# Optimization experiments

Hardware: AMD Instinct MI355X
Metric: run time of the kernel (lower is better)

## Reference

```python
import jax, jax.numpy as jnp
import numpy as np
from jax import lax

B, H, W, C = 8, 64, 64, 256
OUT = 1024          # channels (final conv filters)
KS = 3              # kernel_size
GROUP_DIV = 1
N_GROUPS = C // GROUP_DIV  # 256 -> depthwise-style grouped convs
DN = ('NHWC', 'HWIO', 'NHWC')
EPS = 1e-5


def setup_inputs() -> dict:
    key = jax.random.key(0)
    ks = jax.random.split(key, 6)
    x = jax.random.normal(ks[0], (B, H, W, C), jnp.float32)
    w_spatial = jax.random.normal(ks[1], (B, KS, KS, C // N_GROUPS, C), jnp.float32) * 0.05
    w_pointwise = jax.random.normal(ks[2], (B, 1, 1, C // N_GROUPS, C), jnp.float32) * 0.05
    bias = jax.random.normal(ks[3], (B, C), jnp.float32) * 0.05
    conv_w = jax.random.normal(ks[4], (KS, KS, C, OUT), jnp.float32) * (1.0 / np.sqrt(KS * KS * C))
    conv_b = jnp.zeros((OUT,), jnp.float32)
    return {"x": x, "w_spatial": w_spatial, "w_pointwise": w_pointwise,
            "bias": bias, "conv_w": conv_w, "conv_b": conv_b}


def _instance_norm(x):
    # TF: (x - mean) / (std + eps), population std over H,W per sample/channel
    mean = jnp.mean(x, axis=(1, 2), keepdims=True)
    std = jnp.sqrt(jnp.mean((x - mean) ** 2, axis=(1, 2), keepdims=True))
    return (x - mean) / (std + EPS)


def _per_sample(xi, ws, wp, b):
    # xi: [H,W,C]; ws: [ks,ks,1,C]; wp: [1,1,1,C]; b: [C]
    y = lax.conv_general_dilated(xi[None], ws, (1, 1), 'SAME',
                                 dimension_numbers=DN,
                                 feature_group_count=N_GROUPS)
    y = lax.conv_general_dilated(y, wp, (1, 1), 'VALID',
                                 dimension_numbers=DN,
                                 feature_group_count=N_GROUPS) + b
    return y[0]


def reference(x, w_spatial, w_pointwise, bias, conv_w, conv_b):
    x = _instance_norm(x)
    # batched per-sample dynamic grouped spatial + pointwise conv
    x = jax.vmap(_per_sample)(x, w_spatial, w_pointwise, bias)  # [B,H,W,C]
    # shared 3x3 SAME conv C -> OUT with bias
    y = lax.conv_general_dilated(x, conv_w, (1, 1), 'SAME',
                                 dimension_numbers=DN) + conv_b
    return y
```

## Files before the change

kernel.cpp:

```cpp
#include <hip/hip_runtime.h>
#include <hip/hip_bf16.h>
#include <cstdint>
#include <cstddef>

constexpr int Bn   = 8;
constexpr int Hn   = 64;
constexpr int Wn   = 64;
constexpr int Cn   = 256;
constexpr int OUTC = 1024;
constexpr int HPAD = 66;
constexpr int WPAD = 66;
#define EPS 1e-5f

typedef __attribute__((ext_vector_type(4))) float f32x4;
typedef __bf16 bf16x8 __attribute__((ext_vector_type(8)));

__device__ __forceinline__ void gload_lds16(const void* g, void* l) {
    __builtin_amdgcn_global_load_lds(
        (__attribute__((address_space(1))) void*)g,
        (__attribute__((address_space(3))) void*)l,
        16, 0, 0);
}

__global__ __launch_bounds__(256) void k0_transpose_w(const float* __restrict__ conv_w,
                                                      __hip_bfloat16* __restrict__ wT) {
    __shared__ float tile[64][65];
    const int tap = blockIdx.x;
    const int ct  = blockIdx.y;
    const int ot  = blockIdx.z;
    const int t   = threadIdx.x;
    const int lo  = t & 63;
    const int cq  = t >> 6;

#pragma unroll
    for (int k = 0; k < 16; ++k) {
        int ci = k * 4 + cq;
        tile[lo][ci] = conv_w[((size_t)(tap * Cn + ct * 64 + ci)) * OUTC + ot * 64 + lo];
    }
    __syncthreads();
#pragma unroll
    for (int k = 0; k < 16; ++k) {
        int oo = k * 4 + cq;
        wT[((size_t)(tap * OUTC + ot * 64 + oo)) * Cn + ct * 64 + lo] =
            __float2bfloat16(tile[oo][lo]);
    }
}

__global__ __launch_bounds__(1024) void k1_stats_partial(const float* __restrict__ x,
                                                         float* __restrict__ ps,
                                                         float* __restrict__ pq) {
    __shared__ float sb[2][4][256];
    const int bh = blockIdx.x;
    const int tid = threadIdx.x;
    const int c = tid & 255;
    const int s = tid >> 8;
    const float* row = x + (size_t)bh * Wn * Cn + (size_t)s * 16 * Cn + c;
    float sm = 0.f, q = 0.f;
#pragma unroll
    for (int w = 0; w < 16; ++w) {
        float v = row[(size_t)w * Cn];
        sm += v; q += v * v;
    }
    sb[0][s][c] = sm; sb[1][s][c] = q;
    __syncthreads();
    if (s == 0) {
        float S = 0.f, Q = 0.f;
#pragma unroll
        for (int k = 0; k < 4; ++k) { S += sb[0][k][c]; Q += sb[1][k][c]; }
        ps[bh * Cn + c] = S;
        pq[bh * Cn + c] = Q;
    }
}

__global__ __launch_bounds__(1024) void k2_stats_final(const float* __restrict__ ps,
                                                       const float* __restrict__ pq,
                                                       float* __restrict__ scale,
                                                       float* __restrict__ shift) {
    __shared__ float sb[2][4][256];
    const int b = blockIdx.x;
    const int tid = threadIdx.x;
    const int c = tid & 255;
    const int qd = tid >> 8;
    float S = 0.f, Q = 0.f;
#pragma unroll 4
    for (int i = 0; i < 16; ++i) {
        int h = qd * 16 + i;
        S += ps[(b * Hn + h) * Cn + c];
        Q += pq[(b * Hn + h) * Cn + c];
    }
    sb[0][qd][c] = S; sb[1][qd][c] = Q;
    __syncthreads();
    if (qd == 0) {
        float s2 = 0.f, q2 = 0.f;
#pragma unroll
        for (int k = 0; k < 4; ++k) { s2 += sb[0][k][c]; q2 += sb[1][k][c]; }
        const float inv = 1.f / (float)(Hn * Wn);
        float mean = s2 * inv;
        float var  = fmaxf(q2 * inv - mean * mean, 0.f);
        float sc   = 1.f / (sqrtf(var) + EPS);
        scale[b * Cn + c] = sc;
        shift[b * Cn + c] = -mean * sc;
    }
}

__global__ __launch_bounds__(256) void k3_dwconv(const float* __restrict__ x,
                                                 const float* __restrict__ w_sp,
                                                 const float* __restrict__ w_pw,
                                                 const float* __restrict__ bias,
                                                 const float* __restrict__ scale,
                                                 const float* __restrict__ shift,
                                                 __hip_bfloat16* __restrict__ tpad) {
    const int bq = blockIdx.x;
    const int wq = bq & 3;
    const int bh = bq >> 2;
    const int b  = bh / HPAD;
    const int hp = bh - b * HPAD;
    const int c  = threadIdx.x;
    __hip_bfloat16* orow = tpad + ((size_t)(b * HPAD + hp)) * WPAD * Cn + c;
    const __hip_bfloat16 z = __float2bfloat16(0.f);

    if (hp == 0 || hp == HPAD - 1) {
        int wlo = wq * 17, whi = wlo + 17 < WPAD ? wlo + 17 : WPAD;
        for (int wp = wlo; wp < whi; ++wp) orow[(size_t)wp * Cn] = z;
        return;
    }
    const int h = hp - 1;
    const float sc = scale[b * Cn + c];
    const float sh = shift[b * Cn + c];
    float w9[9];
#pragma unroll
    for (int k = 0; k < 9; ++k) w9[k] = w_sp[(b * 9 + k) * Cn + c];
    const float pw = w_pw[b * Cn + c];
    const float bv = bias[b * Cn + c];
    const float* xb = x + (size_t)b * Hn * Wn * Cn + c;

    bool rv[3];
#pragma unroll
    for (int r = 0; r < 3; ++r) { int rr = h - 1 + r; rv[r] = (rr >= 0 && rr < Hn); }

    if (wq == 0) orow[0] = z;
    if (wq == 3) orow[(size_t)(WPAD - 1) * Cn] = z;

    const int w0 = wq * 16;
    float win[3][3];
#pragma unroll
    for (int r = 0; r < 3; ++r) {
        win[r][0] = (rv[r] && w0 > 0)
                    ? (xb[((size_t)(h - 1 + r) * Wn + (w0 - 1)) * Cn] * sc + sh) : 0.f;
        win[r][1] = rv[r] ? (xb[((size_t)(h - 1 + r) * Wn + w0) * Cn] * sc + sh) : 0.f;
    }
    for (int i = 0; i < 16; ++i) {
        const int w = w0 + i;
#pragma unroll
        for (int r = 0; r < 3; ++r)
            win[r][2] = (rv[r] && (w + 1) < Wn)
                        ? (xb[((size_t)(h - 1 + r) * Wn + (w + 1)) * Cn] * sc + sh) : 0.f;
        float y = 0.f;
#pragma unroll
        for (int r = 0; r < 3; ++r)
#pragma unroll
            for (int qq = 0; qq < 3; ++qq)
                y += win[r][qq] * w9[r * 3 + qq];
        orow[(size_t)(w + 1) * Cn] = __float2bfloat16(y * pw + bv);
#pragma unroll
        for (int r = 0; r < 3; ++r) { win[r][0] = win[r][1]; win[r][1] = win[r][2]; }
    }
}

constexpr int KSTEPS = 72;
constexpr int BUFSZ  = 32768;

__global__ __launch_bounds__(512, 2) void k4_gemm(const __hip_bfloat16* __restrict__ tpad,
                                                  const __hip_bfloat16* __restrict__ wT,
                                                  const float* __restrict__ conv_b,
                                                  float* __restrict__ out) {
    __shared__ __align__(16) char smem[4 * BUFSZ];

    const int tid  = threadIdx.x;
    const int lane = tid & 63;
    const int wv   = tid >> 6;
    const int wm   = wv >> 2;
    const int wn   = wv & 3;
    const int g    = lane >> 4, l15 = lane & 15;

    const int bid = blockIdx.x;
    const int mt  = (bid & 7) * 16 + ((bid >> 3) & 15);
    const int nt  = bid >> 7;
    const int pixbase = mt * 256;
    const int b       = mt >> 4;
    const int hbase   = (mt & 15) * 4;
    const int obase   = nt * 256;

    int aoff[2], boff[2];
#pragma unroll
    for (int j = 0; j < 2; ++j) {
        int u = j * 512 + tid;
        int r = u >> 3, p = u & 7;
        int l = p ^ (r & 7);
        int pix = 2 * r + (l >> 2);
        int hh  = hbase + (pix >> 6);
        int ww  = pix & 63;
        aoff[j] = ((b * HPAD + hh) * WPAD + ww) * Cn + (l & 3) * 8;
        boff[j] = (obase + 2 * r + (l >> 2)) * Cn + (l & 3) * 8;
    }

    auto stageS = [&](int s) {
        const int tap = s >> 3, ks = s & 7;
        const int kh  = tap / 3, kw = tap - 3 * kh;
        const __hip_bfloat16* aS = tpad + ((kh * WPAD + kw) * Cn + ks * 32);
        const __hip_bfloat16* bS = wT + (size_t)tap * (OUTC * Cn) + ks * 32;
        char* buf = smem + (s & 3) * BUFSZ;
        gload_lds16(aS + aoff[0], buf + (size_t)(0 * 512 + wv * 64) * 16);
        gload_lds16(aS + aoff[1], buf + (size_t)(1 * 512 + wv * 64) * 16);
        gload_lds16(bS + boff[0], buf + 16384 + (size_t)(0 * 512 + wv * 64) * 16);
        gload_lds16(bS + boff[1], buf + 16384 + (size_t)(1 * 512 + wv * 64) * 16);
    };

    f32x4 acc[8][4] = {};

    stageS(0);
    stageS(1);

#pragma unroll 1
    for (int t = 0; t < KSTEPS; ++t) {
        if (t < KSTEPS - 1) { asm volatile("s_waitcnt vmcnt(4)" ::: "memory"); }
        else                { asm volatile("s_waitcnt vmcnt(0)" ::: "memory"); }
        __builtin_amdgcn_sched_barrier(0);
        __builtin_amdgcn_s_barrier();
        __builtin_amdgcn_sched_barrier(0);

        char* Ab = smem + (t & 3) * BUFSZ;
        char* Bb = Ab + 16384;

        bf16x8 bfr[4], af[8];
#pragma unroll
        for (int n = 0; n < 4; ++n) {
            int o = wn * 64 + n * 16 + l15;
            int r = o >> 1;
            bfr[n] = *(const bf16x8*)(Bb + r * 128 +
                         ((((o & 1) << 2) | g) ^ (r & 7)) * 16);
        }
#pragma unroll
        for (int m = 0; m < 8; ++m) {
            int pix = wm * 128 + m * 16 + l15;
            int r = pix >> 1;
            af[m] = *(const bf16x8*)(Ab + r * 128 +
                         ((((pix & 1) << 2) | g) ^ (r & 7)) * 16);
        }

        if (t + 2 < KSTEPS) stageS(t + 2);

        __builtin_amdgcn_s_setprio(1);
#pragma unroll
        for (int m = 0; m < 8; ++m)
#pragma unroll
            for (int n = 0; n < 4; ++n)
                acc[m][n] = __builtin_amdgcn_mfma_f32_16x16x32_bf16(
                    af[m], bfr[n], acc[m][n], 0, 0, 0);
        __builtin_amdgcn_s_setprio(0);
    }

    float cb[4];
#pragma unroll
    for (int n = 0; n < 4; ++n) cb[n] = conv_b[obase + wn * 64 + n * 16 + l15];
#pragma unroll
    for (int m = 0; m < 8; ++m) {
#pragma unroll
        for (int j = 0; j < 4; ++j) {
            int r = pixbase + wm * 128 + m * 16 + g * 4 + j;
            float* orow = out + (size_t)r * OUTC + obase + wn * 64 + l15;
#pragma unroll
            for (int n = 0; n < 4; ++n)
                orow[n * 16] = acc[m][n][j] + cb[n];
        }
    }
}

extern "C" void kernel_launch(void* const* d_in, const int* in_sizes, int n_in,
                              void* d_out, int out_size, void* d_ws, size_t ws_size,
                              hipStream_t stream) {
    const float* x      = (const float*)d_in[0];
    const float* w_sp   = (const float*)d_in[1];
    const float* w_pw   = (const float*)d_in[2];
    const float* bias   = (const float*)d_in[3];
    const float* conv_w = (const float*)d_in[4];
    const float* conv_b = (const float*)d_in[5];
    float* out = (float*)d_out;

    char* ws = (char*)d_ws;
    __hip_bfloat16* wT    = (__hip_bfloat16*)(ws);
    float*          ps    = (float*)(ws + 4718592);
    float*          pq    = (float*)(ws + 4718592 + 524288);
    float*          scale = (float*)(ws + 5767168);
    float*          shift = (float*)(ws + 5775360);
    __hip_bfloat16* tpad  = (__hip_bfloat16*)(ws + 5783552);

    k0_transpose_w<<<dim3(9, 4, 16), 256, 0, stream>>>(conv_w, wT);
    k1_stats_partial<<<Bn * Hn, 1024, 0, stream>>>(x, ps, pq);
    k2_stats_final<<<Bn, 1024, 0, stream>>>(ps, pq, scale, shift);
    k3_dwconv<<<Bn * HPAD * 4, 256, 0, stream>>>(x, w_sp, w_pw, bias, scale, shift, tpad);
    k4_gemm<<<512, 512, 0, stream>>>(tpad, wT, conv_b, out);
}
```

Before: 176.5 us.

## Retile implicit-GEMM conv to 128x256 tiles with 4 waves and triple buffering

The main GEMM kernel moves from 256x256 output tiles with 8 waves to 128x256 tiles with 4 waves, each wave computing a 64x128 sub-tile. The grid grows to 1024 blocks. LDS staging drops from four 32KB buffers to three 24KB buffers. The barrier now sits at the end of each iteration, and LDS read addresses are precomputed outside the loop. The aim is a higher MFMA-to-LDS-read ratio per wave, less LDS per block and better occupancy. The cost is more reloading of the A/B tiles across blocks and a shallower prefetch window.

```diff
diff --git a/kernel.cpp b/kernel.cpp
--- a/kernel.cpp
+++ b/kernel.cpp
@@ -168,40 +168,47 @@
 }
 
 constexpr int KSTEPS = 72;
-constexpr int BUFSZ  = 32768;
-
-__global__ __launch_bounds__(512, 2) void k4_gemm(const __hip_bfloat16* __restrict__ tpad,
+constexpr int BUFSZ  = 24576;
+
+__global__ __launch_bounds__(256, 2) void k4_gemm(const __hip_bfloat16* __restrict__ tpad,
                                                   const __hip_bfloat16* __restrict__ wT,
                                                   const float* __restrict__ conv_b,
                                                   float* __restrict__ out) {
-    __shared__ __align__(16) char smem[4 * BUFSZ];
+    __shared__ __align__(16) char smem[3 * BUFSZ];
 
     const int tid  = threadIdx.x;
     const int lane = tid & 63;
     const int wv   = tid >> 6;
-    const int wm   = wv >> 2;
-    const int wn   = wv & 3;
+    const int wm   = wv >> 1;
+    const int wn   = wv & 1;
     const int g    = lane >> 4, l15 = lane & 15;
 
     const int bid = blockIdx.x;
-    const int mt  = (bid & 7) * 16 + ((bid >> 3) & 15);
-    const int nt  = bid >> 7;
-    const int pixbase = mt * 256;
-    const int b       = mt >> 4;
-    const int hbase   = (mt & 15) * 4;
+    const int mt  = (bid & 7) * 32 + ((bid >> 3) & 31);
+    const int nt  = bid >> 8;
+    const int pixbase = mt * 128;
+    const int b       = mt >> 5;
+    const int hbase   = (mt & 31) * 2;
     const int obase   = nt * 256;
 
-    int aoff[2], boff[2];
+    int aoff[2], boff[4];
 #pragma unroll
     for (int j = 0; j < 2; ++j) {
-        int u = j * 512 + tid;
+        int u = j * 256 + tid;
         int r = u >> 3, p = u & 7;
         int l = p ^ (r & 7);
         int pix = 2 * r + (l >> 2);
         int hh  = hbase + (pix >> 6);
         int ww  = pix & 63;
         aoff[j] = ((b * HPAD + hh) * WPAD + ww) * Cn + (l & 3) * 8;
-        boff[j] = (obase + 2 * r + (l >> 2)) * Cn + (l & 3) * 8;
+    }
+#pragma unroll
+    for (int j = 0; j < 4; ++j) {
+        int u = j * 256 + tid;
+        int r = u >> 3, p = u & 7;
+        int l = p ^ (r & 7);
+        int och = 2 * r + (l >> 2);
+        boff[j] = (obase + och) * Cn + (l & 3) * 8;
     }
 
     auto stageS = [&](int s) {
@@ -209,69 +216,69 @@
         const int kh  = tap / 3, kw = tap - 3 * kh;
         const __hip_bfloat16* aS = tpad + ((kh * WPAD + kw) * Cn + ks * 32);
         const __hip_bfloat16* bS = wT + (size_t)tap * (OUTC * Cn) + ks * 32;
-        char* buf = smem + (s & 3) * BUFSZ;
-        gload_lds16(aS + aoff[0], buf + (size_t)(0 * 512 + wv * 64) * 16);
-        gload_lds16(aS + aoff[1], buf + (size_t)(1 * 512 + wv * 64) * 16);
-        gload_lds16(bS + boff[0], buf + 16384 + (size_t)(0 * 512 + wv * 64) * 16);
-        gload_lds16(bS + boff[1], buf + 16384 + (size_t)(1 * 512 + wv * 64) * 16);
+        char* buf = smem + (s % 3) * BUFSZ;
+        gload_lds16(aS + aoff[0], buf + (size_t)(0 * 256 + wv * 64) * 16);
+        gload_lds16(aS + aoff[1], buf + (size_t)(1 * 256 + wv * 64) * 16);
+#pragma unroll
+        for (int j = 0; j < 4; ++j)
+            gload_lds16(bS + boff[j], buf + 8192 + (size_t)(j * 256 + wv * 64) * 16);
     };
 
-    f32x4 acc[8][4] = {};
+    const int slot16 = ((((l15 & 1) << 2) | g) ^ ((l15 >> 1) & 7)) * 16;
+    const int aR = (wm * 32 + (l15 >> 1)) * 128 + slot16;
+    const int bR = 8192 + (wn * 64 + (l15 >> 1)) * 128 + slot16;
+
+    f32x4 acc[4][8] = {};
 
     stageS(0);
     stageS(1);
+    asm volatile("s_waitcnt vmcnt(6)" ::: "memory");
+    __builtin_amdgcn_s_barrier();
+    __builtin_amdgcn_sched_barrier(0);
 
 #pragma unroll 1
     for (int t = 0; t < KSTEPS; ++t) {
-        if (t < KSTEPS - 1) { asm volatile("s_waitcnt vmcnt(4)" ::: "memory"); }
-        else                { asm volatile("s_waitcnt vmcnt(0)" ::: "memory"); }
-        __builtin_amdgcn_sched_barrier(0);
-        __builtin_amdgcn_s_barrier();
-        __builtin_amdgcn_sched_barrier(0);
-
-        char* Ab = smem + (t & 3) * BUFSZ;
-        char* Bb = Ab + 16384;
-
-        bf16x8 bfr[4], af[8];
-#pragma unroll
-        for (int n = 0; n < 4; ++n) {
-            int o = wn * 64 + n * 16 + l15;
-            int r = o >> 1;
-            bfr[n] = *(const bf16x8*)(Bb + r * 128 +
-                         ((((o & 1) << 2) | g) ^ (r & 7)) * 16);
-        }
-#pragma unroll
-        for (int m = 0; m < 8; ++m) {
-            int pix = wm * 128 + m * 16 + l15;
-            int r = pix >> 1;
-            af[m] = *(const bf16x8*)(Ab + r * 128 +
-                         ((((pix & 1) << 2) | g) ^ (r & 7)) * 16);
-        }
+        char* cb = smem + (t % 3) * BUFSZ;
+        bf16x8 bfr[8], af[4];
+#pragma unroll
+        for (int n = 0; n < 8; ++n)
+            bfr[n] = *(const bf16x8*)(cb + bR + n * 1024);
+#pragma unroll
+        for (int m = 0; m < 4; ++m)
+            af[m] = *(const bf16x8*)(cb + aR + m * 1024);
 
         if (t + 2 < KSTEPS) stageS(t + 2);
 
         __builtin_amdgcn_s_setprio(1);
 #pragma unroll
-        for (int m = 0; m < 8; ++m)
-#pragma unroll
-            for (int n = 0; n < 4; ++n)
+        for (int m = 0; m < 4; ++m)
+#pragma unroll
+            for (int n = 0; n < 8; ++n)
                 acc[m][n] = __builtin_amdgcn_mfma_f32_16x16x32_bf16(
                     af[m], bfr[n], acc[m][n], 0, 0, 0);
         __builtin_amdgcn_s_setprio(0);
-    }
-
-    float cb[4];
-#pragma unroll
-    for (int n = 0; n < 4; ++n) cb[n] = conv_b[obase + wn * 64 + n * 16 + l15];
-#pragma unroll
-    for (int m = 0; m < 8; ++m) {
+        __builtin_amdgcn_sched_barrier(0);
+
+        if (t + 1 < KSTEPS) {
+            if (t + 2 < KSTEPS) { asm volatile("s_waitcnt vmcnt(6)" ::: "memory"); }
+            else                { asm volatile("s_waitcnt vmcnt(0)" ::: "memory"); }
+            __builtin_amdgcn_s_barrier();
+            __builtin_amdgcn_sched_barrier(0);
+        }
+    }
+
+    float cb2[8];
+#pragma unroll
+    for (int n = 0; n < 8; ++n) cb2[n] = conv_b[obase + wn * 128 + n * 16 + l15];
+#pragma unroll
+    for (int m = 0; m < 4; ++m) {
 #pragma unroll
         for (int j = 0; j < 4; ++j) {
-            int r = pixbase + wm * 128 + m * 16 + g * 4 + j;
-            float* orow = out + (size_t)r * OUTC + obase + wn * 64 + l15;
-#pragma unroll
-            for (int n = 0; n < 4; ++n)
-                orow[n * 16] = acc[m][n][j] + cb[n];
+            int r = pixbase + wm * 64 + m * 16 + g * 4 + j;
+            float* orow = out + (size_t)r * OUTC + obase + wn * 128 + l15;
+#pragma unroll
+            for (int n = 0; n < 8; ++n)
+                orow[n * 16] = acc[m][n][j] + cb2[n];
         }
     }
 }
@@ -299,5 +306,5 @@
     k1_stats_partial<<<Bn * Hn, 1024, 0, stream>>>(x, ps, pq);
     k2_stats_final<<<Bn, 1024, 0, stream>>>(ps, pq, scale, shift);
     k3_dwconv<<<Bn * HPAD * 4, 256, 0, stream>>>(x, w_sp, w_pw, bias, scale, shift, tpad);
-    k4_gemm<<<512, 512, 0, stream>>>(tpad, wT, conv_b, out);
-}
+    k4_gemm<<<1024, 256, 0, stream>>>(tpad, wT, conv_b, out);
+}
```

New measurement: 177.6 us. Within noise of the previous version (+0.6%).
